# Kernel tuning notes

Measured on AMD Instinct MI355X. Metric: run time of the kernel, lower is better.

## Reference

```python
import jax, jax.numpy as jnp
import numpy as np

B, N, C = 1, 256, 128        # batch, n_res, norm_channel
H, AC = 4, 32                # num_head, attention_channel


def setup_inputs() -> dict:
    key = jax.random.key(0)
    ks = jax.random.split(key, 9)
    s = 0.02
    return {
        "act": jax.random.normal(ks[0], (B, N, N, C), jnp.float32),
        "mask": jnp.ones((B, N, N), jnp.float32),
        "ln_g": jnp.ones((C,), jnp.float32),
        "ln_b": jnp.zeros((C,), jnp.float32),
        "wq": (jax.random.normal(ks[1], (C, H * AC), jnp.float32) * s),
        "wk": (jax.random.normal(ks[2], (C, H * AC), jnp.float32) * s),
        "wv": (jax.random.normal(ks[3], (C, H * AC), jnp.float32) * s),
        "w2d": (jax.random.normal(ks[4], (C, H), jnp.float32) * s),
        "wg": (jax.random.normal(ks[5], (C, H * AC), jnp.float32) * s),
        "bg": jnp.zeros((H * AC,), jnp.float32),
        "wo": (jax.random.normal(ks[6], (H * AC, C), jnp.float32) * s),
        "bo": jnp.zeros((C,), jnp.float32),
    }


def reference(act, mask, ln_g, ln_b, wq, wk, wv, w2d, wg, bg, wo, bo):
    eps = 1e-5
    mu = jnp.mean(act, axis=-1, keepdims=True)
    var = jnp.mean(jnp.square(act - mu), axis=-1, keepdims=True)
    a = (act - mu) * jax.lax.rsqrt(var + eps) * ln_g + ln_b  # LayerNorm

    b_, m_, i_, _ = a.shape
    q = (a @ wq).reshape(b_, m_, i_, H, AC)
    k = (a @ wk).reshape(b_, m_, i_, H, AC)
    v = (a @ wv).reshape(b_, m_, i_, H, AC)

    factor = 1.0 / np.sqrt(AC).astype(np.float32)
    # mask bias: [b, m, 1, 1, j]
    bias = (1e9 * (mask - 1.0))[:, :, None, None, :]
    aff = jnp.einsum('bmihc,bmjhc->bmhij', q * factor, k) + bias

    # pair bias: [b, h, i, j], broadcast over m (torch trailing-dim broadcast, b=1)
    nb = jnp.einsum('bijc,ch->bhij', a, w2d)
    weights = jax.nn.softmax(aff + nb[:, None], axis=-1)  # [b,m,h,i,j]

    g = jax.nn.sigmoid(a @ wg + bg).reshape(b_, m_, i_, H, AC)
    out = jnp.einsum('bmhqk,bmkhc->bmqhc', weights, v) * g  # [b,m,q,h,c]
    return out.reshape(b_, m_, i_, H * AC) @ wo + bo
```

## Files before the change

### kernel.cpp

```cpp
#include <hip/hip_runtime.h>
#include <hip/hip_fp16.h>
#include <math.h>


#define NRES 256
#define CCH  128
#define NROWS (NRES * NRES)
#define FACTOR 0.17677669529663687f

typedef __attribute__((ext_vector_type(8))) __bf16 bf16x8;
typedef __attribute__((ext_vector_type(4))) float f32x4;

__device__ __forceinline__ f32x4 mfma16(bf16x8 a, bf16x8 b, f32x4 c) {
    return __builtin_amdgcn_mfma_f32_16x16x32_bf16(a, b, c, 0, 0, 0);
}

union PK4 { __bf16 b[4]; uint2 u2; };

__device__ __forceinline__ void hilo(float x, __bf16& h, __bf16& l) {
    h = (__bf16)x;
    l = (__bf16)(x - (float)h);
}

__global__ __launch_bounds__(256) void prep_kernel(
    const float* __restrict__ wq, const float* __restrict__ wk,
    const float* __restrict__ wv, const float* __restrict__ wg,
    const float* __restrict__ wo,
    __bf16* __restrict__ wph, __bf16* __restrict__ wpl)
{
    const int gid = blockIdx.x * 256 + threadIdx.x;
    const int wid = gid >> 11;
    const int rem = gid & 2047;
    const int nstrip = rem >> 8;
    const int kf = (rem >> 6) & 3;
    const int lane = rem & 63;
    const int l15 = lane & 15, quad = lane >> 4;
    const float* W = (wid == 0) ? wq : (wid == 1) ? wk :
                     (wid == 2) ? wv : (wid == 3) ? wg : wo;
    const float scale = (wid == 0) ? FACTOR : 1.0f;
    bf16x8 hb, lb;
    #pragma unroll
    for (int e = 0; e < 8; ++e) {
        int k = kf * 32 + quad * 8 + e;
        int n = nstrip * 16 + l15;
        float v = W[k * CCH + n] * scale;
        __bf16 h, l; hilo(v, h, l);
        hb[e] = h; lb[e] = l;
    }
    *(bf16x8*)&wph[(size_t)gid * 8] = hb;
    *(bf16x8*)&wpl[(size_t)gid * 8] = lb;
}

__global__ __launch_bounds__(256) void nb_kernel(
    const float* __restrict__ act, const float* __restrict__ ln_g,
    const float* __restrict__ ln_b, const float* __restrict__ w2d,
    float* __restrict__ nbP)
{
    const int t = threadIdx.x, w = t >> 6, lane = t & 63;
    const int r0w = blockIdx.x * 128 + w * 32;
    const int row = lane >> 1, half = lane & 1;
    const int grow = r0w + row;
    const float* __restrict__ xp = act + (size_t)grow * CCH + half * 64;
    float4 x4[16];
    #pragma unroll
    for (int c = 0; c < 16; ++c) x4[c] = *(const float4*)(xp + c * 4);
    float s = 0.f, sq = 0.f;
    #pragma unroll
    for (int c = 0; c < 16; ++c) {
        s  += (x4[c].x + x4[c].y) + (x4[c].z + x4[c].w);
        sq += x4[c].x * x4[c].x + x4[c].y * x4[c].y +
              x4[c].z * x4[c].z + x4[c].w * x4[c].w;
    }
    s  += __shfl_xor(s, 1, 64);
    sq += __shfl_xor(sq, 1, 64);
    float mu  = s * (1.0f / CCH);
    float var = fmaf(sq, 1.0f / CCH, -mu * mu);
    float rs  = rsqrtf(var + 1e-5f);
    float nb[4] = {0.f, 0.f, 0.f, 0.f};
    const float4* __restrict__ w2d4 = (const float4*)w2d;
    #pragma unroll
    for (int c = 0; c < 16; ++c) {
        float4 g4 = *(const float4*)&ln_g[half * 64 + c * 4];
        float4 b4 = *(const float4*)&ln_b[half * 64 + c * 4];
        float* xv = (float*)&x4[c];
        float* gv = (float*)&g4;
        float* bv = (float*)&b4;
        #pragma unroll
        for (int e = 0; e < 4; ++e) {
            float av = fmaf((xv[e] - mu) * rs, gv[e], bv[e]);
            float4 wv = w2d4[half * 64 + c * 4 + e];
            nb[0] = fmaf(av, wv.x, nb[0]);
            nb[1] = fmaf(av, wv.y, nb[1]);
            nb[2] = fmaf(av, wv.z, nb[2]);
            nb[3] = fmaf(av, wv.w, nb[3]);
        }
    }
    #pragma unroll
    for (int hh = 0; hh < 4; ++hh)
        nb[hh] += __shfl_xor(nb[hh], 1, 64);
    if (half == 0) {
        const int i = grow >> 8, j = grow & 255;
        #pragma unroll
        for (int hh = 0; hh < 4; ++hh) {
            size_t f = ((size_t)hh << 14) + ((size_t)(i >> 4) << 10) +
                       ((size_t)(j >> 4) << 6) + ((size_t)((j >> 2) & 3) << 4) +
                       (i & 15);
            nbP[f * 4 + (j & 3)] = nb[hh];
        }
    }
}

__device__ __forceinline__ void proj32(const bf16x8* A0, const bf16x8* A1,
    const __bf16* __restrict__ Bh, int lane, f32x4* acc0, f32x4* acc1)
{
    #pragma unroll
    for (int n = 0; n < 8; ++n) {
        acc0[n] = (f32x4){0.f, 0.f, 0.f, 0.f};
        acc1[n] = (f32x4){0.f, 0.f, 0.f, 0.f};
    }
    #pragma unroll
    for (int kf = 0; kf < 4; ++kf)
        #pragma unroll
        for (int n = 0; n < 8; ++n) {
            bf16x8 bh = *(const bf16x8*)&Bh[(size_t)((n * 4 + kf) * 64 + lane) * 8];
            acc0[n] = mfma16(A0[kf], bh, acc0[n]);
            acc1[n] = mfma16(A1[kf], bh, acc1[n]);
        }
}

__global__ __launch_bounds__(512) void mega_kernel(
    const float* __restrict__ act, const float* __restrict__ ln_g,
    const float* __restrict__ ln_b, const __bf16* __restrict__ wph,
    const __bf16* __restrict__ wpl, const float* __restrict__ bg,
    const float* __restrict__ mask, const float* __restrict__ nbP,
    const float* __restrict__ bo, float* __restrict__ out)
{
    __shared__ __align__(16) char smem[148480];
    const int t = threadIdx.x, w = t >> 6, lane = t & 63;
    const int l15 = lane & 15, quad = lane >> 4;
    const int m = blockIdx.x;
    __bf16* const Kl = (__bf16*)smem;
    __bf16* const aH = (__bf16*)(smem + w * 8704);
    __bf16* const VT = (__bf16*)(smem + 69632);
    __bf16* const ph = (__bf16*)(smem + 137216 + w * 1280);
    float*  const biasrow = (float*)(smem + 147456);

    if (t < 256) biasrow[t] = 1e9f * (mask[m * NRES + t] - 1.0f);

    {
        const int row = lane >> 1, half = lane & 1;
        const int grow = m * NRES + w * 32 + row;
        const float* __restrict__ xp = act + (size_t)grow * CCH + half * 64;
        float4 x4[16];
        #pragma unroll
        for (int c = 0; c < 16; ++c) x4[c] = *(const float4*)(xp + c * 4);
        float s = 0.f, sq = 0.f;
        #pragma unroll
        for (int c = 0; c < 16; ++c) {
            s  += (x4[c].x + x4[c].y) + (x4[c].z + x4[c].w);
            sq += x4[c].x * x4[c].x + x4[c].y * x4[c].y +
                  x4[c].z * x4[c].z + x4[c].w * x4[c].w;
        }
        s  += __shfl_xor(s, 1, 64);
        sq += __shfl_xor(sq, 1, 64);
        float mu  = s * (1.0f / CCH);
        float var = fmaf(sq, 1.0f / CCH, -mu * mu);
        float rs  = rsqrtf(var + 1e-5f);
        #pragma unroll
        for (int c2 = 0; c2 < 8; ++c2) {
            bf16x8 pk;
            #pragma unroll
            for (int cc = 0; cc < 2; ++cc) {
                const int c = c2 * 2 + cc;
                float4 g4 = *(const float4*)&ln_g[half * 64 + c * 4];
                float4 b4 = *(const float4*)&ln_b[half * 64 + c * 4];
                float* xv = (float*)&x4[c];
                float* gv = (float*)&g4;
                float* bv = (float*)&b4;
                #pragma unroll
                for (int e = 0; e < 4; ++e)
                    pk[cc * 4 + e] = (__bf16)fmaf((xv[e] - mu) * rs, gv[e], bv[e]);
            }
            *(bf16x8*)&aH[row * 136 + half * 64 + c2 * 8] = pk;
        }
    }

    bf16x8 A0[4], A1[4];
    #pragma unroll
    for (int kf = 0; kf < 4; ++kf) {
        const int ao = l15 * 136 + kf * 32 + quad * 8;
        A0[kf] = *(const bf16x8*)&aH[ao];
        A1[kf] = *(const bf16x8*)&aH[ao + 16 * 136];
    }

    f32x4 acc0[8], acc1[8];
    bf16x8 Qh[4][2];
    uint2  greg[4][2][2];

    proj32(A0, A1, wph, lane, acc0, acc1);
    {
        __bf16* const sth = aH;
        #pragma unroll
        for (int sp = 0; sp < 2; ++sp) {
            f32x4* accp = sp ? acc1 : acc0;
            #pragma unroll
            for (int n = 0; n < 8; ++n)
                #pragma unroll
                for (int r = 0; r < 4; ++r)
                    sth[(quad * 4 + r) * 136 + n * 16 + l15] = (__bf16)accp[n][r];
            #pragma unroll
            for (int h = 0; h < 4; ++h)
                Qh[h][sp] = *(const bf16x8*)&sth[l15 * 136 + h * 32 + quad * 8];
        }
    }

    proj32(A0, A1, wph + 3 * 16384, lane, acc0, acc1);
    {
        __half* const sthH = (__half*)aH;
        #pragma unroll
        for (int sp = 0; sp < 2; ++sp) {
            f32x4* accp = sp ? acc1 : acc0;
            #pragma unroll
            for (int n = 0; n < 8; ++n)
                #pragma unroll
                for (int r = 0; r < 4; ++r) {
                    float v = accp[n][r] + bg[n * 16 + l15];
                    sthH[(quad * 4 + r) * 136 + n * 16 + l15] =
                        (__half)(1.0f / (1.0f + __expf(-v)));
                }
            #pragma unroll
            for (int h = 0; h < 4; ++h)
                #pragma unroll
                for (int c = 0; c < 2; ++c)
                    greg[h][sp][c] =
                        *(const uint2*)&sthH[l15 * 136 + h * 32 + c * 16 + quad * 4];
        }
    }

    proj32(A0, A1, wph + 1 * 16384, lane, acc0, acc1);
    {
        __bf16* const Kp = aH;
        #pragma unroll
        for (int sp = 0; sp < 2; ++sp) {
            f32x4* accp = sp ? acc1 : acc0;
            #pragma unroll
            for (int n = 0; n < 8; ++n)
                #pragma unroll
                for (int r = 0; r < 4; ++r)
                    Kp[(sp * 16 + quad * 4 + r) * 136 + n * 16 + l15] =
                        (__bf16)accp[n][r];
        }
    }

    proj32(A0, A1, wph + 2 * 16384, lane, acc0, acc1);
    {
        const int jbase = w * 32;
        #pragma unroll
        for (int sp = 0; sp < 2; ++sp) {
            f32x4* accp = sp ? acc1 : acc0;
            #pragma unroll
            for (int n = 0; n < 8; ++n)
                #pragma unroll
                for (int r = 0; r < 4; ++r)
                    VT[(n * 16 + l15) * 264 + jbase + sp * 16 + quad * 4 + r] =
                        (__bf16)accp[n][r];
        }
    }
    __syncthreads();

    uint2 ovh[4][2][2], ovl[4][2][2];
    #pragma unroll
    for (int h = 0; h < 4; ++h) {
        f32x4 O[2][2];
        float ls[2] = {0.f, 0.f};
        #pragma unroll
        for (int s = 0; s < 2; ++s) {
            O[s][0] = (f32x4){0.f, 0.f, 0.f, 0.f};
            O[s][1] = (f32x4){0.f, 0.f, 0.f, 0.f};
        }
        #pragma unroll 1
        for (int jb = 0; jb < NRES; jb += 32) {
            bf16x8 Kh[2];
            #pragma unroll
            for (int js = 0; js < 2; ++js)
                Kh[js] = *(const bf16x8*)&Kl[(jb + js * 16 + l15) * 136 +
                                             h * 32 + quad * 8];
            bf16x8 Vh2[2];
            #pragma unroll
            for (int c = 0; c < 2; ++c)
                Vh2[c] = *(const bf16x8*)&VT[(h * 32 + c * 16 + l15) * 264 +
                                             jb + quad * 8];
            #pragma unroll
            for (int s = 0; s < 2; ++s) {
                #pragma unroll
                for (int js = 0; js < 2; ++js) {
                    f32x4 S = (f32x4){0.f, 0.f, 0.f, 0.f};
                    S = mfma16(Kh[js], Qh[h][s], S);
                    size_t f4 = (size_t)h * 16384 + (size_t)(w * 2 + s) * 1024 +
                                (size_t)((jb >> 4) + js) * 64 + quad * 16 + l15;
                    float4 nb4 = *(const float4*)&nbP[f4 * 4];
                    float4 mb4 = *(const float4*)&biasrow[jb + js * 16 + quad * 4];
                    float p0 = __expf(S[0] + nb4.x + mb4.x - 4.0f);
                    float p1 = __expf(S[1] + nb4.y + mb4.y - 4.0f);
                    float p2 = __expf(S[2] + nb4.z + mb4.z - 4.0f);
                    float p3 = __expf(S[3] + nb4.w + mb4.w - 4.0f);
                    ls[s] += (p0 + p1) + (p2 + p3);
                    PK4 hh;
                    hh.b[0] = (__bf16)p0; hh.b[1] = (__bf16)p1;
                    hh.b[2] = (__bf16)p2; hh.b[3] = (__bf16)p3;
                    *(uint2*)&ph[l15 * 40 + js * 16 + quad * 4] = hh.u2;
                }
                bf16x8 Ph = *(const bf16x8*)&ph[l15 * 40 + quad * 8];
                #pragma unroll
                for (int c = 0; c < 2; ++c)
                    O[s][c] = mfma16(Vh2[c], Ph, O[s][c]);
            }
        }
        #pragma unroll
        for (int s = 0; s < 2; ++s) {
            ls[s] += __shfl_xor(ls[s], 16, 64);
            ls[s] += __shfl_xor(ls[s], 32, 64);
        }
        #pragma unroll
        for (int s = 0; s < 2; ++s) {
            float inv = 1.0f / ls[s];
            #pragma unroll
            for (int c = 0; c < 2; ++c) {
                const __half* gh = (const __half*)&greg[h][s][c];
                PK4 hh, lo;
                #pragma unroll
                for (int r = 0; r < 4; ++r) {
                    float v = O[s][c][r] * inv * (float)gh[r];
                    __bf16 hb; __bf16 lb; hilo(v, hb, lb);
                    hh.b[r] = hb; lo.b[r] = lb;
                }
                ovh[h][s][c] = hh.u2;
                ovl[h][s][c] = lo.u2;
            }
        }
    }
    __syncthreads();

    {
        __bf16* const sth = aH;
        #pragma unroll
        for (int h = 0; h < 4; ++h)
            #pragma unroll
            for (int s = 0; s < 2; ++s)
                #pragma unroll
                for (int c = 0; c < 2; ++c)
                    *(uint2*)&sth[(s * 16 + l15) * 136 + h * 32 + c * 16 + quad * 4] =
                        ovh[h][s][c];
        bf16x8 Ah0[4], Ah1[4];
        #pragma unroll
        for (int kf = 0; kf < 4; ++kf) {
            Ah0[kf] = *(const bf16x8*)&sth[l15 * 136 + kf * 32 + quad * 8];
            Ah1[kf] = *(const bf16x8*)&sth[(16 + l15) * 136 + kf * 32 + quad * 8];
        }
        #pragma unroll
        for (int h = 0; h < 4; ++h)
            #pragma unroll
            for (int s = 0; s < 2; ++s)
                #pragma unroll
                for (int c = 0; c < 2; ++c)
                    *(uint2*)&sth[(s * 16 + l15) * 136 + h * 32 + c * 16 + quad * 4] =
                        ovl[h][s][c];
        bf16x8 Al0[4], Al1[4];
        #pragma unroll
        for (int kf = 0; kf < 4; ++kf) {
            Al0[kf] = *(const bf16x8*)&sth[l15 * 136 + kf * 32 + quad * 8];
            Al1[kf] = *(const bf16x8*)&sth[(16 + l15) * 136 + kf * 32 + quad * 8];
        }

        const __bf16* __restrict__ Bh = wph + (size_t)4 * 16384;
        const __bf16* __restrict__ Bl = wpl + (size_t)4 * 16384;
        #pragma unroll
        for (int n = 0; n < 8; ++n) {
            acc0[n] = (f32x4){0.f, 0.f, 0.f, 0.f};
            acc1[n] = (f32x4){0.f, 0.f, 0.f, 0.f};
        }
        #pragma unroll
        for (int kf = 0; kf < 4; ++kf)
            #pragma unroll
            for (int n = 0; n < 8; ++n) {
                size_t boff = (size_t)((n * 4 + kf) * 64 + lane) * 8;
                bf16x8 bh = *(const bf16x8*)&Bh[boff];
                bf16x8 bl = *(const bf16x8*)&Bl[boff];
                acc0[n] = mfma16(Ah0[kf], bh, acc0[n]);
                acc0[n] = mfma16(Ah0[kf], bl, acc0[n]);
                acc0[n] = mfma16(Al0[kf], bh, acc0[n]);
                acc1[n] = mfma16(Ah1[kf], bh, acc1[n]);
                acc1[n] = mfma16(Ah1[kf], bl, acc1[n]);
                acc1[n] = mfma16(Al1[kf], bh, acc1[n]);
            }

        const size_t rbase = (size_t)m * NRES + w * 32;
        #pragma unroll
        for (int n = 0; n < 8; ++n) {
            float b = bo[n * 16 + l15];
            #pragma unroll
            for (int r = 0; r < 4; ++r) {
                out[(rbase + quad * 4 + r) * CCH + n * 16 + l15] = acc0[n][r] + b;
                out[(rbase + 16 + quad * 4 + r) * CCH + n * 16 + l15] = acc1[n][r] + b;
            }
        }
    }
}

extern "C" void kernel_launch(void* const* d_in, const int* in_sizes, int n_in,
                              void* d_out, int out_size, void* d_ws, size_t ws_size,
                              hipStream_t stream)
{
    const float* act  = (const float*)d_in[0];
    const float* mask = (const float*)d_in[1];
    const float* ln_g = (const float*)d_in[2];
    const float* ln_b = (const float*)d_in[3];
    const float* wq   = (const float*)d_in[4];
    const float* wk   = (const float*)d_in[5];
    const float* wv   = (const float*)d_in[6];
    const float* w2d  = (const float*)d_in[7];
    const float* wg   = (const float*)d_in[8];
    const float* bg   = (const float*)d_in[9];
    const float* wo   = (const float*)d_in[10];
    const float* bo   = (const float*)d_in[11];
    float* out = (float*)d_out;

    float* nbP = (float*)d_ws;
    __bf16* wph = (__bf16*)(nbP + 4 * NROWS);
    __bf16* wpl = wph + 5 * 16384;

    prep_kernel<<<40, 256, 0, stream>>>(wq, wk, wv, wg, wo, wph, wpl);
    nb_kernel<<<512, 256, 0, stream>>>(act, ln_g, ln_b, w2d, nbP);
    mega_kernel<<<256, 512, 0, stream>>>(
        act, ln_g, ln_b, wph, wpl, bg, mask, nbP, bo, out);
}
```

Measured before the change: 193.8 us.

## Fuse pair-bias computation into mega kernel with cooperative grid sync

```diff
diff --git a/kernel.cpp b/kernel.cpp
--- a/kernel.cpp
+++ b/kernel.cpp
@@ -1,6 +1,9 @@
 #include <hip/hip_runtime.h>
 #include <hip/hip_fp16.h>
+#include <hip/hip_cooperative_groups.h>
 #include <math.h>
+
+namespace cg = cooperative_groups;
 
 
 #define NRES 256
@@ -51,65 +54,6 @@
     *(bf16x8*)&wpl[(size_t)gid * 8] = lb;
 }
 
-__global__ __launch_bounds__(256) void nb_kernel(
-    const float* __restrict__ act, const float* __restrict__ ln_g,
-    const float* __restrict__ ln_b, const float* __restrict__ w2d,
-    float* __restrict__ nbP)
-{
-    const int t = threadIdx.x, w = t >> 6, lane = t & 63;
-    const int r0w = blockIdx.x * 128 + w * 32;
-    const int row = lane >> 1, half = lane & 1;
-    const int grow = r0w + row;
-    const float* __restrict__ xp = act + (size_t)grow * CCH + half * 64;
-    float4 x4[16];
-    #pragma unroll
-    for (int c = 0; c < 16; ++c) x4[c] = *(const float4*)(xp + c * 4);
-    float s = 0.f, sq = 0.f;
-    #pragma unroll
-    for (int c = 0; c < 16; ++c) {
-        s  += (x4[c].x + x4[c].y) + (x4[c].z + x4[c].w);
-        sq += x4[c].x * x4[c].x + x4[c].y * x4[c].y +
-              x4[c].z * x4[c].z + x4[c].w * x4[c].w;
-    }
-    s  += __shfl_xor(s, 1, 64);
-    sq += __shfl_xor(sq, 1, 64);
-    float mu  = s * (1.0f / CCH);
-    float var = fmaf(sq, 1.0f / CCH, -mu * mu);
-    float rs  = rsqrtf(var + 1e-5f);
-    float nb[4] = {0.f, 0.f, 0.f, 0.f};
-    const float4* __restrict__ w2d4 = (const float4*)w2d;
-    #pragma unroll
-    for (int c = 0; c < 16; ++c) {
-        float4 g4 = *(const float4*)&ln_g[half * 64 + c * 4];
-        float4 b4 = *(const float4*)&ln_b[half * 64 + c * 4];
-        float* xv = (float*)&x4[c];
-        float* gv = (float*)&g4;
-        float* bv = (float*)&b4;
-        #pragma unroll
-        for (int e = 0; e < 4; ++e) {
-            float av = fmaf((xv[e] - mu) * rs, gv[e], bv[e]);
-            float4 wv = w2d4[half * 64 + c * 4 + e];
-            nb[0] = fmaf(av, wv.x, nb[0]);
-            nb[1] = fmaf(av, wv.y, nb[1]);
-            nb[2] = fmaf(av, wv.z, nb[2]);
-            nb[3] = fmaf(av, wv.w, nb[3]);
-        }
-    }
-    #pragma unroll
-    for (int hh = 0; hh < 4; ++hh)
-        nb[hh] += __shfl_xor(nb[hh], 1, 64);
-    if (half == 0) {
-        const int i = grow >> 8, j = grow & 255;
-        #pragma unroll
-        for (int hh = 0; hh < 4; ++hh) {
-            size_t f = ((size_t)hh << 14) + ((size_t)(i >> 4) << 10) +
-                       ((size_t)(j >> 4) << 6) + ((size_t)((j >> 2) & 3) << 4) +
-                       (i & 15);
-            nbP[f * 4 + (j & 3)] = nb[hh];
-        }
-    }
-}
-
 __device__ __forceinline__ void proj32(const bf16x8* A0, const bf16x8* A1,
     const __bf16* __restrict__ Bh, int lane, f32x4* acc0, f32x4* acc1)
 {
@@ -130,10 +74,11 @@
 
 __global__ __launch_bounds__(512) void mega_kernel(
     const float* __restrict__ act, const float* __restrict__ ln_g,
-    const float* __restrict__ ln_b, const __bf16* __restrict__ wph,
-    const __bf16* __restrict__ wpl, const float* __restrict__ bg,
-    const float* __restrict__ mask, const float* __restrict__ nbP,
-    const float* __restrict__ bo, float* __restrict__ out)
+    const float* __restrict__ ln_b, const float* __restrict__ w2d,
+    const __bf16* __restrict__ wph, const __bf16* __restrict__ wpl,
+    const float* __restrict__ bg, const float* __restrict__ mask,
+    float* __restrict__ nbP, const float* __restrict__ bo,
+    float* __restrict__ out)
 {
     __shared__ __align__(16) char smem[148480];
     const int t = threadIdx.x, w = t >> 6, lane = t & 63;
@@ -166,6 +111,8 @@
         float mu  = s * (1.0f / CCH);
         float var = fmaf(sq, 1.0f / CCH, -mu * mu);
         float rs  = rsqrtf(var + 1e-5f);
+        float nb[4] = {0.f, 0.f, 0.f, 0.f};
+        const float4* __restrict__ w2d4 = (const float4*)w2d;
         #pragma unroll
         for (int c2 = 0; c2 < 8; ++c2) {
             bf16x8 pk;
@@ -178,10 +125,30 @@
                 float* gv = (float*)&g4;
                 float* bv = (float*)&b4;
                 #pragma unroll
-                for (int e = 0; e < 4; ++e)
-                    pk[cc * 4 + e] = (__bf16)fmaf((xv[e] - mu) * rs, gv[e], bv[e]);
+                for (int e = 0; e < 4; ++e) {
+                    float av = fmaf((xv[e] - mu) * rs, gv[e], bv[e]);
+                    pk[cc * 4 + e] = (__bf16)av;
+                    float4 wv = w2d4[half * 64 + c * 4 + e];
+                    nb[0] = fmaf(av, wv.x, nb[0]);
+                    nb[1] = fmaf(av, wv.y, nb[1]);
+                    nb[2] = fmaf(av, wv.z, nb[2]);
+                    nb[3] = fmaf(av, wv.w, nb[3]);
+                }
             }
             *(bf16x8*)&aH[row * 136 + half * 64 + c2 * 8] = pk;
+        }
+        #pragma unroll
+        for (int hh = 0; hh < 4; ++hh)
+            nb[hh] += __shfl_xor(nb[hh], 1, 64);
+        if (half == 0) {
+            const int i = grow >> 8, j = grow & 255;
+            #pragma unroll
+            for (int hh = 0; hh < 4; ++hh) {
+                size_t f = ((size_t)hh << 14) + ((size_t)(i >> 4) << 10) +
+                           ((size_t)(j >> 4) << 6) + ((size_t)((j >> 2) & 3) << 4) +
+                           (i & 15);
+                nbP[f * 4 + (j & 3)] = nb[hh];
+            }
         }
     }
 
@@ -267,6 +234,8 @@
         }
     }
     __syncthreads();
+    __threadfence();
+    cg::this_grid().sync();
 
     uint2 ovh[4][2][2], ovl[4][2][2];
     #pragma unroll
@@ -278,6 +247,14 @@
             O[s][0] = (f32x4){0.f, 0.f, 0.f, 0.f};
             O[s][1] = (f32x4){0.f, 0.f, 0.f, 0.f};
         }
+        float4 nb_a[2][2], nb_b[2][2];
+        #pragma unroll
+        for (int s = 0; s < 2; ++s)
+            #pragma unroll
+            for (int js = 0; js < 2; ++js)
+                nb_a[s][js] = *(const float4*)&nbP[
+                    ((size_t)h * 16384 + (size_t)(w * 2 + s) * 1024 +
+                     (size_t)js * 64 + quad * 16 + l15) * 4];
         #pragma unroll 1
         for (int jb = 0; jb < NRES; jb += 32) {
             bf16x8 Kh[2];
@@ -290,15 +267,21 @@
             for (int c = 0; c < 2; ++c)
                 Vh2[c] = *(const bf16x8*)&VT[(h * 32 + c * 16 + l15) * 264 +
                                              jb + quad * 8];
+            const int jn = (jb + 32 < NRES) ? (jb >> 4) + 2 : 0;
+            #pragma unroll
+            for (int s = 0; s < 2; ++s)
+                #pragma unroll
+                for (int js = 0; js < 2; ++js)
+                    nb_b[s][js] = *(const float4*)&nbP[
+                        ((size_t)h * 16384 + (size_t)(w * 2 + s) * 1024 +
+                         (size_t)(jn + js) * 64 + quad * 16 + l15) * 4];
             #pragma unroll
             for (int s = 0; s < 2; ++s) {
                 #pragma unroll
                 for (int js = 0; js < 2; ++js) {
                     f32x4 S = (f32x4){0.f, 0.f, 0.f, 0.f};
                     S = mfma16(Kh[js], Qh[h][s], S);
-                    size_t f4 = (size_t)h * 16384 + (size_t)(w * 2 + s) * 1024 +
-                                (size_t)((jb >> 4) + js) * 64 + quad * 16 + l15;
-                    float4 nb4 = *(const float4*)&nbP[f4 * 4];
+                    float4 nb4 = nb_a[s][js];
                     float4 mb4 = *(const float4*)&biasrow[jb + js * 16 + quad * 4];
                     float p0 = __expf(S[0] + nb4.x + mb4.x - 4.0f);
                     float p1 = __expf(S[1] + nb4.y + mb4.y - 4.0f);
@@ -315,6 +298,11 @@
                 for (int c = 0; c < 2; ++c)
                     O[s][c] = mfma16(Vh2[c], Ph, O[s][c]);
             }
+            #pragma unroll
+            for (int s = 0; s < 2; ++s)
+                #pragma unroll
+                for (int js = 0; js < 2; ++js)
+                    nb_a[s][js] = nb_b[s][js];
         }
         #pragma unroll
         for (int s = 0; s < 2; ++s) {
@@ -430,7 +418,12 @@
     __bf16* wpl = wph + 5 * 16384;
 
     prep_kernel<<<40, 256, 0, stream>>>(wq, wk, wv, wg, wo, wph, wpl);
-    nb_kernel<<<512, 256, 0, stream>>>(act, ln_g, ln_b, w2d, nbP);
-    mega_kernel<<<256, 512, 0, stream>>>(
-        act, ln_g, ln_b, wph, wpl, bg, mask, nbP, bo, out);
-}
+
+    void* kargs[] = {
+        (void*)&act, (void*)&ln_g, (void*)&ln_b, (void*)&w2d,
+        (void*)&wph, (void*)&wpl, (void*)&bg, (void*)&mask,
+        (void*)&nbP, (void*)&bo, (void*)&out
+    };
+    hipLaunchCooperativeKernel((void*)mega_kernel, dim3(256), dim3(512),
+                               kargs, 0, stream);
+}
```

Result: slower. 270.4 us (+39.5%).

## Use 1024-thread blocks with 16 rows per wave, exp2 softmax, fused prep kernels

Applied to the files above, without the earlier changes.

```diff
diff --git a/kernel.cpp b/kernel.cpp
--- a/kernel.cpp
+++ b/kernel.cpp
@@ -7,6 +7,7 @@
 #define CCH  128
 #define NROWS (NRES * NRES)
 #define FACTOR 0.17677669529663687f
+#define LOG2E  1.44269504088896341f
 
 typedef __attribute__((ext_vector_type(8))) __bf16 bf16x8;
 typedef __attribute__((ext_vector_type(4))) float f32x4;
@@ -22,41 +23,41 @@
     l = (__bf16)(x - (float)h);
 }
 
-__global__ __launch_bounds__(256) void prep_kernel(
+__global__ __launch_bounds__(256) void nbprep_kernel(
+    const float* __restrict__ act, const float* __restrict__ ln_g,
+    const float* __restrict__ ln_b, const float* __restrict__ w2d,
     const float* __restrict__ wq, const float* __restrict__ wk,
     const float* __restrict__ wv, const float* __restrict__ wg,
     const float* __restrict__ wo,
-    __bf16* __restrict__ wph, __bf16* __restrict__ wpl)
-{
-    const int gid = blockIdx.x * 256 + threadIdx.x;
-    const int wid = gid >> 11;
-    const int rem = gid & 2047;
-    const int nstrip = rem >> 8;
-    const int kf = (rem >> 6) & 3;
-    const int lane = rem & 63;
-    const int l15 = lane & 15, quad = lane >> 4;
-    const float* W = (wid == 0) ? wq : (wid == 1) ? wk :
-                     (wid == 2) ? wv : (wid == 3) ? wg : wo;
-    const float scale = (wid == 0) ? FACTOR : 1.0f;
-    bf16x8 hb, lb;
-    #pragma unroll
-    for (int e = 0; e < 8; ++e) {
-        int k = kf * 32 + quad * 8 + e;
-        int n = nstrip * 16 + l15;
-        float v = W[k * CCH + n] * scale;
-        __bf16 h, l; hilo(v, h, l);
-        hb[e] = h; lb[e] = l;
-    }
-    *(bf16x8*)&wph[(size_t)gid * 8] = hb;
-    *(bf16x8*)&wpl[(size_t)gid * 8] = lb;
-}
-
-__global__ __launch_bounds__(256) void nb_kernel(
-    const float* __restrict__ act, const float* __restrict__ ln_g,
-    const float* __restrict__ ln_b, const float* __restrict__ w2d,
+    __bf16* __restrict__ wph, __bf16* __restrict__ wpl,
     float* __restrict__ nbP)
 {
-    const int t = threadIdx.x, w = t >> 6, lane = t & 63;
+    const int t = threadIdx.x;
+    if (blockIdx.x >= 512) {
+        const int gid = (blockIdx.x - 512) * 256 + t;
+        const int wid = gid >> 11;
+        const int rem = gid & 2047;
+        const int nstrip = rem >> 8;
+        const int kf = (rem >> 6) & 3;
+        const int lane = rem & 63;
+        const int l15 = lane & 15, quad = lane >> 4;
+        const float* W = (wid == 0) ? wq : (wid == 1) ? wk :
+                         (wid == 2) ? wv : (wid == 3) ? wg : wo;
+        const float scale = (wid == 0) ? FACTOR * LOG2E : 1.0f;
+        bf16x8 hb, lb;
+        #pragma unroll
+        for (int e = 0; e < 8; ++e) {
+            int k = kf * 32 + quad * 8 + e;
+            int n = nstrip * 16 + l15;
+            float v = W[k * CCH + n] * scale;
+            __bf16 h, l; hilo(v, h, l);
+            hb[e] = h; lb[e] = l;
+        }
+        *(bf16x8*)&wph[(size_t)gid * 8] = hb;
+        *(bf16x8*)&wpl[(size_t)gid * 8] = lb;
+        return;
+    }
+    const int w = t >> 6, lane = t & 63;
     const int r0w = blockIdx.x * 128 + w * 32;
     const int row = lane >> 1, half = lane & 1;
     const int grow = r0w + row;
@@ -105,75 +106,75 @@
             size_t f = ((size_t)hh << 14) + ((size_t)(i >> 4) << 10) +
                        ((size_t)(j >> 4) << 6) + ((size_t)((j >> 2) & 3) << 4) +
                        (i & 15);
-            nbP[f * 4 + (j & 3)] = nb[hh];
-        }
-    }
-}
-
-__device__ __forceinline__ void proj32(const bf16x8* A0, const bf16x8* A1,
-    const __bf16* __restrict__ Bh, int lane, f32x4* acc0, f32x4* acc1)
+            nbP[f * 4 + (j & 3)] = nb[hh] * LOG2E;
+        }
+    }
+}
+
+__device__ __forceinline__ void proj16(const bf16x8* A0,
+    const __bf16* __restrict__ Bh, int lane, f32x4* acc)
 {
     #pragma unroll
-    for (int n = 0; n < 8; ++n) {
-        acc0[n] = (f32x4){0.f, 0.f, 0.f, 0.f};
-        acc1[n] = (f32x4){0.f, 0.f, 0.f, 0.f};
-    }
+    for (int n = 0; n < 8; ++n) acc[n] = (f32x4){0.f, 0.f, 0.f, 0.f};
     #pragma unroll
     for (int kf = 0; kf < 4; ++kf)
         #pragma unroll
         for (int n = 0; n < 8; ++n) {
             bf16x8 bh = *(const bf16x8*)&Bh[(size_t)((n * 4 + kf) * 64 + lane) * 8];
-            acc0[n] = mfma16(A0[kf], bh, acc0[n]);
-            acc1[n] = mfma16(A1[kf], bh, acc1[n]);
-        }
-}
-
-__global__ __launch_bounds__(512) void mega_kernel(
+            acc[n] = mfma16(A0[kf], bh, acc[n]);
+        }
+}
+
+__global__ __launch_bounds__(1024) void mega_kernel(
     const float* __restrict__ act, const float* __restrict__ ln_g,
     const float* __restrict__ ln_b, const __bf16* __restrict__ wph,
     const __bf16* __restrict__ wpl, const float* __restrict__ bg,
     const float* __restrict__ mask, const float* __restrict__ nbP,
     const float* __restrict__ bo, float* __restrict__ out)
 {
-    __shared__ __align__(16) char smem[148480];
+    __shared__ __align__(16) char smem[158720];
     const int t = threadIdx.x, w = t >> 6, lane = t & 63;
     const int l15 = lane & 15, quad = lane >> 4;
     const int m = blockIdx.x;
     __bf16* const Kl = (__bf16*)smem;
-    __bf16* const aH = (__bf16*)(smem + w * 8704);
+    __bf16* const aH = (__bf16*)(smem + w * 4352);
     __bf16* const VT = (__bf16*)(smem + 69632);
     __bf16* const ph = (__bf16*)(smem + 137216 + w * 1280);
-    float*  const biasrow = (float*)(smem + 147456);
-
-    if (t < 256) biasrow[t] = 1e9f * (mask[m * NRES + t] - 1.0f);
+    float*  const biasrow = (float*)(smem + 157696);
+
+    if (t < 256)
+        biasrow[t] = fmaf(1.442695e9f, mask[m * NRES + t] - 1.0f, -4.0f * LOG2E);
 
     {
-        const int row = lane >> 1, half = lane & 1;
-        const int grow = m * NRES + w * 32 + row;
-        const float* __restrict__ xp = act + (size_t)grow * CCH + half * 64;
-        float4 x4[16];
-        #pragma unroll
-        for (int c = 0; c < 16; ++c) x4[c] = *(const float4*)(xp + c * 4);
+        const int row = lane >> 2, g = lane & 3;
+        const int grow = m * NRES + w * 16 + row;
+        const float* __restrict__ xp = act + (size_t)grow * CCH + g * 32;
+        float4 x4[8];
+        #pragma unroll
+        for (int c = 0; c < 8; ++c) x4[c] = *(const float4*)(xp + c * 4);
         float s = 0.f, sq = 0.f;
         #pragma unroll
-        for (int c = 0; c < 16; ++c) {
+        for (int c = 0; c < 8; ++c) {
             s  += (x4[c].x + x4[c].y) + (x4[c].z + x4[c].w);
             sq += x4[c].x * x4[c].x + x4[c].y * x4[c].y +
                   x4[c].z * x4[c].z + x4[c].w * x4[c].w;
         }
-        s  += __shfl_xor(s, 1, 64);
-        sq += __shfl_xor(sq, 1, 64);
+        #pragma unroll
+        for (int o = 1; o <= 2; o <<= 1) {
+            s  += __shfl_xor(s, o, 64);
+            sq += __shfl_xor(sq, o, 64);
+        }
         float mu  = s * (1.0f / CCH);
         float var = fmaf(sq, 1.0f / CCH, -mu * mu);
         float rs  = rsqrtf(var + 1e-5f);
         #pragma unroll
-        for (int c2 = 0; c2 < 8; ++c2) {
+        for (int c2 = 0; c2 < 4; ++c2) {
             bf16x8 pk;
             #pragma unroll
             for (int cc = 0; cc < 2; ++cc) {
                 const int c = c2 * 2 + cc;
-                float4 g4 = *(const float4*)&ln_g[half * 64 + c * 4];
-                float4 b4 = *(const float4*)&ln_b[half * 64 + c * 4];
+                float4 g4 = *(const float4*)&ln_g[g * 32 + c * 4];
+                float4 b4 = *(const float4*)&ln_b[g * 32 + c * 4];
                 float* xv = (float*)&x4[c];
                 float* gv = (float*)&g4;
                 float* bv = (float*)&b4;
@@ -181,103 +182,80 @@
                 for (int e = 0; e < 4; ++e)
                     pk[cc * 4 + e] = (__bf16)fmaf((xv[e] - mu) * rs, gv[e], bv[e]);
             }
-            *(bf16x8*)&aH[row * 136 + half * 64 + c2 * 8] = pk;
-        }
-    }
-
-    bf16x8 A0[4], A1[4];
-    #pragma unroll
-    for (int kf = 0; kf < 4; ++kf) {
-        const int ao = l15 * 136 + kf * 32 + quad * 8;
-        A0[kf] = *(const bf16x8*)&aH[ao];
-        A1[kf] = *(const bf16x8*)&aH[ao + 16 * 136];
-    }
-
-    f32x4 acc0[8], acc1[8];
-    bf16x8 Qh[4][2];
-    uint2  greg[4][2][2];
-
-    proj32(A0, A1, wph, lane, acc0, acc1);
+            *(bf16x8*)&aH[row * 136 + g * 32 + c2 * 8] = pk;
+        }
+    }
+
+    bf16x8 A0[4];
+    #pragma unroll
+    for (int kf = 0; kf < 4; ++kf)
+        A0[kf] = *(const bf16x8*)&aH[l15 * 136 + kf * 32 + quad * 8];
+
+    f32x4 acc[8];
+    bf16x8 Qh[4];
+    uint2  greg[4][2];
+
+    proj16(A0, wph, lane, acc);
     {
         __bf16* const sth = aH;
         #pragma unroll
-        for (int sp = 0; sp < 2; ++sp) {
-            f32x4* accp = sp ? acc1 : acc0;
-            #pragma unroll
-            for (int n = 0; n < 8; ++n)
-                #pragma unroll
-                for (int r = 0; r < 4; ++r)
-                    sth[(quad * 4 + r) * 136 + n * 16 + l15] = (__bf16)accp[n][r];
-            #pragma unroll
-            for (int h = 0; h < 4; ++h)
-                Qh[h][sp] = *(const bf16x8*)&sth[l15 * 136 + h * 32 + quad * 8];
-        }
-    }
-
-    proj32(A0, A1, wph + 3 * 16384, lane, acc0, acc1);
+        for (int n = 0; n < 8; ++n)
+            #pragma unroll
+            for (int r = 0; r < 4; ++r)
+                sth[(quad * 4 + r) * 136 + n * 16 + l15] = (__bf16)acc[n][r];
+        #pragma unroll
+        for (int h = 0; h < 4; ++h)
+            Qh[h] = *(const bf16x8*)&sth[l15 * 136 + h * 32 + quad * 8];
+    }
+
+    proj16(A0, wph + 3 * 16384, lane, acc);
     {
         __half* const sthH = (__half*)aH;
         #pragma unroll
-        for (int sp = 0; sp < 2; ++sp) {
-            f32x4* accp = sp ? acc1 : acc0;
-            #pragma unroll
-            for (int n = 0; n < 8; ++n)
-                #pragma unroll
-                for (int r = 0; r < 4; ++r) {
-                    float v = accp[n][r] + bg[n * 16 + l15];
-                    sthH[(quad * 4 + r) * 136 + n * 16 + l15] =
-                        (__half)(1.0f / (1.0f + __expf(-v)));
-                }
-            #pragma unroll
-            for (int h = 0; h < 4; ++h)
-                #pragma unroll
-                for (int c = 0; c < 2; ++c)
-                    greg[h][sp][c] =
-                        *(const uint2*)&sthH[l15 * 136 + h * 32 + c * 16 + quad * 4];
-        }
-    }
-
-    proj32(A0, A1, wph + 1 * 16384, lane, acc0, acc1);
-    {
-        __bf16* const Kp = aH;
-        #pragma unroll
-        for (int sp = 0; sp < 2; ++sp) {
-            f32x4* accp = sp ? acc1 : acc0;
-            #pragma unroll
-            for (int n = 0; n < 8; ++n)
-                #pragma unroll
-                for (int r = 0; r < 4; ++r)
-                    Kp[(sp * 16 + quad * 4 + r) * 136 + n * 16 + l15] =
-                        (__bf16)accp[n][r];
-        }
-    }
-
-    proj32(A0, A1, wph + 2 * 16384, lane, acc0, acc1);
-    {
-        const int jbase = w * 32;
-        #pragma unroll
-        for (int sp = 0; sp < 2; ++sp) {
-            f32x4* accp = sp ? acc1 : acc0;
-            #pragma unroll
-            for (int n = 0; n < 8; ++n)
-                #pragma unroll
-                for (int r = 0; r < 4; ++r)
-                    VT[(n * 16 + l15) * 264 + jbase + sp * 16 + quad * 4 + r] =
-                        (__bf16)accp[n][r];
-        }
-    }
+        for (int n = 0; n < 8; ++n)
+            #pragma unroll
+            for (int r = 0; r < 4; ++r) {
+                float v = acc[n][r] + bg[n * 16 + l15];
+                sthH[(quad * 4 + r) * 136 + n * 16 + l15] =
+                    (__half)(1.0f / (1.0f + __expf(-v)));
+            }
+        #pragma unroll
+        for (int h = 0; h < 4; ++h)
+            #pragma unroll
+            for (int c = 0; c < 2; ++c)
+                greg[h][c] =
+                    *(const uint2*)&sthH[l15 * 136 + h * 32 + c * 16 + quad * 4];
+    }
+
+    proj16(A0, wph + 1 * 16384, lane, acc);
+    #pragma unroll
+    for (int n = 0; n < 8; ++n)
+        #pragma unroll
+        for (int r = 0; r < 4; ++r)
+            aH[(quad * 4 + r) * 136 + n * 16 + l15] = (__bf16)acc[n][r];
+
+    proj16(A0, wph + 2 * 16384, lane, acc);
+    #pragma unroll
+    for (int n = 0; n < 8; ++n)
+        #pragma unroll
+        for (int r = 0; r < 4; ++r)
+            VT[(n * 16 + l15) * 264 + w * 16 + quad * 4 + r] = (__bf16)acc[n][r];
+
     __syncthreads();
 
-    uint2 ovh[4][2][2], ovl[4][2][2];
+    uint2 ovh[4][2], ovl[4][2];
     #pragma unroll
     for (int h = 0; h < 4; ++h) {
-        f32x4 O[2][2];
-        float ls[2] = {0.f, 0.f};
-        #pragma unroll
-        for (int s = 0; s < 2; ++s) {
-            O[s][0] = (f32x4){0.f, 0.f, 0.f, 0.f};
-            O[s][1] = (f32x4){0.f, 0.f, 0.f, 0.f};
-        }
+        f32x4 O[2];
+        O[0] = (f32x4){0.f, 0.f, 0.f, 0.f};
+        O[1] = (f32x4){0.f, 0.f, 0.f, 0.f};
+        float ls = 0.f;
+        float4 nb_a[2], nb_b[2];
+        #pragma unroll
+        for (int js = 0; js < 2; ++js)
+            nb_a[js] = *(const float4*)&nbP[
+                ((size_t)h * 16384 + (size_t)w * 1024 +
+                 (size_t)js * 64 + quad * 16 + l15) * 4];
         #pragma unroll 1
         for (int jb = 0; jb < NRES; jb += 32) {
             bf16x8 Kh[2];
@@ -290,53 +268,50 @@
             for (int c = 0; c < 2; ++c)
                 Vh2[c] = *(const bf16x8*)&VT[(h * 32 + c * 16 + l15) * 264 +
                                              jb + quad * 8];
-            #pragma unroll
-            for (int s = 0; s < 2; ++s) {
-                #pragma unroll
-                for (int js = 0; js < 2; ++js) {
-                    f32x4 S = (f32x4){0.f, 0.f, 0.f, 0.f};
-                    S = mfma16(Kh[js], Qh[h][s], S);
-                    size_t f4 = (size_t)h * 16384 + (size_t)(w * 2 + s) * 1024 +
-                                (size_t)((jb >> 4) + js) * 64 + quad * 16 + l15;
-                    float4 nb4 = *(const float4*)&nbP[f4 * 4];
-                    float4 mb4 = *(const float4*)&biasrow[jb + js * 16 + quad * 4];
-                    float p0 = __expf(S[0] + nb4.x + mb4.x - 4.0f);
-                    float p1 = __expf(S[1] + nb4.y + mb4.y - 4.0f);
-                    float p2 = __expf(S[2] + nb4.z + mb4.z - 4.0f);
-                    float p3 = __expf(S[3] + nb4.w + mb4.w - 4.0f);
-                    ls[s] += (p0 + p1) + (p2 + p3);
-                    PK4 hh;
-                    hh.b[0] = (__bf16)p0; hh.b[1] = (__bf16)p1;
-                    hh.b[2] = (__bf16)p2; hh.b[3] = (__bf16)p3;
-                    *(uint2*)&ph[l15 * 40 + js * 16 + quad * 4] = hh.u2;
-                }
-                bf16x8 Ph = *(const bf16x8*)&ph[l15 * 40 + quad * 8];
-                #pragma unroll
-                for (int c = 0; c < 2; ++c)
-                    O[s][c] = mfma16(Vh2[c], Ph, O[s][c]);
-            }
-        }
-        #pragma unroll
-        for (int s = 0; s < 2; ++s) {
-            ls[s] += __shfl_xor(ls[s], 16, 64);
-            ls[s] += __shfl_xor(ls[s], 32, 64);
-        }
-        #pragma unroll
-        for (int s = 0; s < 2; ++s) {
-            float inv = 1.0f / ls[s];
-            #pragma unroll
-            for (int c = 0; c < 2; ++c) {
-                const __half* gh = (const __half*)&greg[h][s][c];
-                PK4 hh, lo;
-                #pragma unroll
-                for (int r = 0; r < 4; ++r) {
-                    float v = O[s][c][r] * inv * (float)gh[r];
-                    __bf16 hb; __bf16 lb; hilo(v, hb, lb);
-                    hh.b[r] = hb; lo.b[r] = lb;
-                }
-                ovh[h][s][c] = hh.u2;
-                ovl[h][s][c] = lo.u2;
-            }
+            const int jn = (jb + 32 < NRES) ? (jb >> 4) + 2 : 0;
+            #pragma unroll
+            for (int js = 0; js < 2; ++js)
+                nb_b[js] = *(const float4*)&nbP[
+                    ((size_t)h * 16384 + (size_t)w * 1024 +
+                     (size_t)(jn + js) * 64 + quad * 16 + l15) * 4];
+            #pragma unroll
+            for (int js = 0; js < 2; ++js) {
+                f32x4 S = (f32x4){0.f, 0.f, 0.f, 0.f};
+                S = mfma16(Kh[js], Qh[h], S);
+                float4 nb4 = nb_a[js];
+                float4 mb4 = *(const float4*)&biasrow[jb + js * 16 + quad * 4];
+                float p0 = exp2f(S[0] + nb4.x + mb4.x);
+                float p1 = exp2f(S[1] + nb4.y + mb4.y);
+                float p2 = exp2f(S[2] + nb4.z + mb4.z);
+                float p3 = exp2f(S[3] + nb4.w + mb4.w);
+                ls += (p0 + p1) + (p2 + p3);
+                PK4 hh;
+                hh.b[0] = (__bf16)p0; hh.b[1] = (__bf16)p1;
+                hh.b[2] = (__bf16)p2; hh.b[3] = (__bf16)p3;
+                *(uint2*)&ph[l15 * 40 + js * 16 + quad * 4] = hh.u2;
+            }
+            bf16x8 Ph = *(const bf16x8*)&ph[l15 * 40 + quad * 8];
+            #pragma unroll
+            for (int c = 0; c < 2; ++c)
+                O[c] = mfma16(Vh2[c], Ph, O[c]);
+            nb_a[0] = nb_b[0];
+            nb_a[1] = nb_b[1];
+        }
+        ls += __shfl_xor(ls, 16, 64);
+        ls += __shfl_xor(ls, 32, 64);
+        float inv = 1.0f / ls;
+        #pragma unroll
+        for (int c = 0; c < 2; ++c) {
+            const __half* gh = (const __half*)&greg[h][c];
+            PK4 hh, lo;
+            #pragma unroll
+            for (int r = 0; r < 4; ++r) {
+                float v = O[c][r] * inv * (float)gh[r];
+                __bf16 hb; __bf16 lb; hilo(v, hb, lb);
+                hh.b[r] = hb; lo.b[r] = lb;
+            }
+            ovh[h][c] = hh.u2;
+            ovl[h][c] = lo.u2;
         }
     }
     __syncthreads();
@@ -346,39 +321,26 @@
         #pragma unroll
         for (int h = 0; h < 4; ++h)
             #pragma unroll
-            for (int s = 0; s < 2; ++s)
-                #pragma unroll
-                for (int c = 0; c < 2; ++c)
-                    *(uint2*)&sth[(s * 16 + l15) * 136 + h * 32 + c * 16 + quad * 4] =
-                        ovh[h][s][c];
-        bf16x8 Ah0[4], Ah1[4];
-        #pragma unroll
-        for (int kf = 0; kf < 4; ++kf) {
+            for (int c = 0; c < 2; ++c)
+                *(uint2*)&sth[l15 * 136 + h * 32 + c * 16 + quad * 4] = ovh[h][c];
+        bf16x8 Ah0[4];
+        #pragma unroll
+        for (int kf = 0; kf < 4; ++kf)
             Ah0[kf] = *(const bf16x8*)&sth[l15 * 136 + kf * 32 + quad * 8];
-            Ah1[kf] = *(const bf16x8*)&sth[(16 + l15) * 136 + kf * 32 + quad * 8];
-        }
         #pragma unroll
         for (int h = 0; h < 4; ++h)
             #pragma unroll
-            for (int s = 0; s < 2; ++s)
-                #pragma unroll
-                for (int c = 0; c < 2; ++c)
-                    *(uint2*)&sth[(s * 16 + l15) * 136 + h * 32 + c * 16 + quad * 4] =
-                        ovl[h][s][c];
-        bf16x8 Al0[4], Al1[4];
-        #pragma unroll
-        for (int kf = 0; kf < 4; ++kf) {
+            for (int c = 0; c < 2; ++c)
+                *(uint2*)&sth[l15 * 136 + h * 32 + c * 16 + quad * 4] = ovl[h][c];
+        bf16x8 Al0[4];
+        #pragma unroll
+        for (int kf = 0; kf < 4; ++kf)
             Al0[kf] = *(const bf16x8*)&sth[l15 * 136 + kf * 32 + quad * 8];
-            Al1[kf] = *(const bf16x8*)&sth[(16 + l15) * 136 + kf * 32 + quad * 8];
-        }
 
         const __bf16* __restrict__ Bh = wph + (size_t)4 * 16384;
         const __bf16* __restrict__ Bl = wpl + (size_t)4 * 16384;
         #pragma unroll
-        for (int n = 0; n < 8; ++n) {
-            acc0[n] = (f32x4){0.f, 0.f, 0.f, 0.f};
-            acc1[n] = (f32x4){0.f, 0.f, 0.f, 0.f};
-        }
+        for (int n = 0; n < 8; ++n) acc[n] = (f32x4){0.f, 0.f, 0.f, 0.f};
         #pragma unroll
         for (int kf = 0; kf < 4; ++kf)
             #pragma unroll
@@ -386,23 +348,18 @@
                 size_t boff = (size_t)((n * 4 + kf) * 64 + lane) * 8;
                 bf16x8 bh = *(const bf16x8*)&Bh[boff];
                 bf16x8 bl = *(const bf16x8*)&Bl[boff];
-                acc0[n] = mfma16(Ah0[kf], bh, acc0[n]);
-                acc0[n] = mfma16(Ah0[kf], bl, acc0[n]);
-                acc0[n] = mfma16(Al0[kf], bh, acc0[n]);
-                acc1[n] = mfma16(Ah1[kf], bh, acc1[n]);
-                acc1[n] = mfma16(Ah1[kf], bl, acc1[n]);
-                acc1[n] = mfma16(Al1[kf], bh, acc1[n]);
-            }
-
-        const size_t rbase = (size_t)m * NRES + w * 32;
+                acc[n] = mfma16(Ah0[kf], bh, acc[n]);
+                acc[n] = mfma16(Ah0[kf], bl, acc[n]);
+                acc[n] = mfma16(Al0[kf], bh, acc[n]);
+            }
+
+        const size_t rbase = (size_t)m * NRES + w * 16;
         #pragma unroll
         for (int n = 0; n < 8; ++n) {
             float b = bo[n * 16 + l15];
             #pragma unroll
-            for (int r = 0; r < 4; ++r) {
-                out[(rbase + quad * 4 + r) * CCH + n * 16 + l15] = acc0[n][r] + b;
-                out[(rbase + 16 + quad * 4 + r) * CCH + n * 16 + l15] = acc1[n][r] + b;
-            }
+            for (int r = 0; r < 4; ++r)
+                out[(rbase + quad * 4 + r) * CCH + n * 16 + l15] = acc[n][r] + b;
         }
     }
 }
@@ -429,8 +386,8 @@
     __bf16* wph = (__bf16*)(nbP + 4 * NROWS);
     __bf16* wpl = wph + 5 * 16384;
 
-    prep_kernel<<<40, 256, 0, stream>>>(wq, wk, wv, wg, wo, wph, wpl);
-    nb_kernel<<<512, 256, 0, stream>>>(act, ln_g, ln_b, w2d, nbP);
-    mega_kernel<<<256, 512, 0, stream>>>(
+    nbprep_kernel<<<552, 256, 0, stream>>>(
+        act, ln_g, ln_b, w2d, wq, wk, wv, wg, wo, wph, wpl, nbP);
+    mega_kernel<<<256, 1024, 0, stream>>>(
         act, ln_g, ln_b, wph, wpl, bg, mask, nbP, bo, out);
 }
```

Measured after the change: 193.6 us. No clear change (-0.1%).
